# Optimization experiments

Measured on AMD Instinct MI355X. Metric: run time of the kernel, lower is better.

The kernel has to match this reference:

```python
import jax, jax.numpy as jnp
import numpy as np

B, S, E = 2, 2048, 1024
H, W_SIZE = 16, 128
D = E // H


def setup_inputs() -> dict:
    key = jax.random.key(0)
    ks = jax.random.split(key, 7)
    std = 1.0 / np.sqrt(E)
    return {
        "x": jax.random.normal(ks[0], (B, S, E), dtype=jnp.float32),
        "Wq": jax.random.normal(ks[1], (E, E), dtype=jnp.float32) * std,
        "bq": jax.random.normal(ks[2], (E,), dtype=jnp.float32) * std,
        "Wk": jax.random.normal(ks[3], (E, E), dtype=jnp.float32) * std,
        "bk": jax.random.normal(ks[4], (E,), dtype=jnp.float32) * std,
        "Wv": jax.random.normal(ks[5], (E, E), dtype=jnp.float32) * std,
        "bv": jax.random.normal(ks[6], (E,), dtype=jnp.float32) * std,
    }


def reference(x, Wq, bq, Wk, bk, Wv, bv):
    b, s, e = x.shape
    scale = jnp.float32(D) ** -0.5
    # torch Linear: y = x @ W.T + b
    # Faithful to original: view() splits [b, s, e] -> [b, H, s, D] WITHOUT transpose
    q = (x @ Wq.T + bq).reshape(b, H, s, D)
    k = (x @ Wk.T + bk).reshape(b, H, s, D)
    v = (x @ Wv.T + bv).reshape(b, H, s, D)
    # window: scores kept for j in [max(0, i - w), min(s, i + w)), zeros elsewhere
    i = jnp.arange(s)[:, None]
    j = jnp.arange(s)[None, :]
    mask = (j >= i - W_SIZE) & (j < i + W_SIZE)  # [s, s]
    qk = jnp.einsum("bhid,bhjd->bhij", q, k)
    # out-of-window entries are ZERO (not -inf) and softmax is over the full row,
    # exactly matching the original zero-padded score tensor.
    scores = jnp.where(mask, qk, 0.0) * scale
    probs = jax.nn.softmax(scores, axis=-1)
    out = jnp.einsum("bhij,bhjd->bhid", probs, v)  # [b, H, s, D]
    out = out.transpose(0, 2, 1, 3).reshape(b, s, e)
    return out
```

## Files before the change

### kernel.cpp

```cpp
#include <hip/hip_runtime.h>
#include <math.h>

#define S_LEN 2048
#define E_DIM 1024
#define NHEAD 16
#define HD 64
#define WIN 128
#define NB 2
#define MTOT (NB * S_LEN)
#define NMAT 3072

typedef float f32x4 __attribute__((ext_vector_type(4)));
typedef short bf16x8 __attribute__((ext_vector_type(8)));

#define GLOAD_LDS(g, l) __builtin_amdgcn_global_load_lds( \
    (const __attribute__((address_space(1))) unsigned int*)(g), \
    (__attribute__((address_space(3))) unsigned int*)(l), 16, 0, 0)

__device__ __forceinline__ unsigned short f2bf(float f) {
    unsigned u = __float_as_uint(f);
    u += 0x7fffu + ((u >> 16) & 1u);
    return (unsigned short)(u >> 16);
}
__device__ __forceinline__ float bf2f(unsigned short u) {
    return __uint_as_float(((unsigned)u) << 16);
}

__global__ __launch_bounds__(256) void convert_kernel(
    const float* __restrict__ x, const float* __restrict__ wq,
    const float* __restrict__ wk, const float* __restrict__ wv,
    unsigned short* __restrict__ xb, unsigned short* __restrict__ wb)
{
    const int NXQ = MTOT * E_DIM / 4;
    const int NWQ = E_DIM * E_DIM / 4;
    const int TOT = NXQ + 3 * NWQ;
    for (int i = blockIdx.x * 256 + threadIdx.x; i < TOT; i += gridDim.x * 256) {
        const float* src; unsigned short* dst; int off;
        if (i < NXQ)               { src = x;  dst = xb;                     off = i; }
        else if (i < NXQ + NWQ)    { src = wq; dst = wb;                     off = i - NXQ; }
        else if (i < NXQ + 2*NWQ)  { src = wk; dst = wb + E_DIM * E_DIM;     off = i - NXQ - NWQ; }
        else                       { src = wv; dst = wb + 2 * E_DIM * E_DIM; off = i - NXQ - 2*NWQ; }
        float4 v = ((const float4*)src)[off];
        ushort4 o;
        o.x = f2bf(v.x); o.y = f2bf(v.y); o.z = f2bf(v.z); o.w = f2bf(v.w);
        ((ushort4*)dst)[off] = o;
    }
}

__global__ __launch_bounds__(256) void gemm_mfma(
    const unsigned short* __restrict__ Ab, const unsigned short* __restrict__ Bb,
    const float* __restrict__ bq, const float* __restrict__ bk, const float* __restrict__ bv,
    unsigned short* __restrict__ Qb, unsigned short* __restrict__ Kb,
    unsigned short* __restrict__ Vb)
{
    __shared__ __align__(256) unsigned short As[128 * 64];
    __shared__ __align__(256) unsigned short Bs[128 * 64];
    const int tid  = threadIdx.x;
    const int lane = tid & 63;
    const int w    = tid >> 6;
    const int wm   = w & 1, wn = w >> 1;
    const int m0   = blockIdx.y * 128;
    const int n0   = blockIdx.x * 128;
    const int l15  = lane & 15, l4 = lane >> 4;

    f32x4 acc[16] = {};

    for (int k0 = 0; k0 < E_DIM; k0 += 64) {
        #pragma unroll
        for (int is = 0; is < 4; ++is) {
            int gid = is * 256 + tid;
            int r = gid >> 3, sl = gid & 7;
            int gran = sl ^ (r & 7);
            int wbs = is * 256 + (tid & 192);
            GLOAD_LDS(Ab + (size_t)(m0 + r) * E_DIM + k0 + gran * 8, As + wbs * 8);
            GLOAD_LDS(Bb + (size_t)(n0 + r) * E_DIM + k0 + gran * 8, Bs + wbs * 8);
        }
        __syncthreads();
        #pragma unroll
        for (int kk = 0; kk < 2; ++kk) {
            bf16x8 af[4], bfr[4];
            int sa = (kk * 4 + l4) ^ (l15 & 7);
            #pragma unroll
            for (int t = 0; t < 4; ++t) {
                int ra = wm * 64 + t * 16 + l15;
                af[t]  = *(const bf16x8*)&As[ra * 64 + sa * 8];
                int rb = wn * 64 + t * 16 + l15;
                bfr[t] = *(const bf16x8*)&Bs[rb * 64 + sa * 8];
            }
            #pragma unroll
            for (int mt = 0; mt < 4; ++mt)
                #pragma unroll
                for (int nt = 0; nt < 4; ++nt)
                    acc[mt * 4 + nt] = __builtin_amdgcn_mfma_f32_16x16x32_bf16(
                        af[mt], bfr[nt], acc[mt * 4 + nt], 0, 0, 0);
        }
        __syncthreads();
    }

    const int sel = n0 >> 10;
    const float* bias = (sel == 0) ? bq : ((sel == 1) ? bk : bv);
    unsigned short* Yb = (sel == 0) ? Qb : ((sel == 1) ? Kb : Vb);
    const int nbase = (n0 & 1023) + wn * 64;
    #pragma unroll
    for (int mt = 0; mt < 4; ++mt) {
        #pragma unroll
        for (int nt = 0; nt < 4; ++nt) {
            int n = nbase + nt * 16 + l15;
            int c = n >> 6, d = n & 63;
            float bb = bias[n];
            #pragma unroll
            for (int r = 0; r < 4; ++r) {
                int m = m0 + wm * 64 + mt * 16 + l4 * 4 + r;
                int b = m >> 11, s = m & 2047;
                int h = s >> 7;
                int i = ((s & 127) << 4) + c;
                Yb[(((size_t)(b * 16 + h) * S_LEN + i) << 6) + d] =
                    f2bf(acc[mt * 4 + nt][r] + bb);
            }
        }
    }
}

__global__ __launch_bounds__(256) void vtot_part_kernel(
    const unsigned short* __restrict__ Vb, float* __restrict__ vtp)
{
    const int bh = blockIdx.x, seg = blockIdx.y;
    const int d = threadIdx.x & 63, sl = threadIdx.x >> 6;
    const unsigned short* p = Vb + ((size_t)bh * S_LEN + seg * 256 + sl * 64) * HD + d;
    float s = 0.f;
    #pragma unroll 8
    for (int j = 0; j < 64; ++j) s += bf2f(p[(size_t)j * HD]);
    __shared__ float red[4][64];
    red[sl][d] = s;
    __syncthreads();
    if (sl == 0)
        vtp[(seg * NB * NHEAD + bh) * HD + d] = red[0][d] + red[1][d] + red[2][d] + red[3][d];
}

__global__ __launch_bounds__(256) void attn_mfma(
    const unsigned short* __restrict__ Qb, const unsigned short* __restrict__ Kb,
    const unsigned short* __restrict__ Vb, const float* __restrict__ vtp,
    float* __restrict__ out)
{
    __shared__ __align__(256) unsigned short qps[9216];
    __shared__ __align__(256) unsigned short ks[2][64 * 64];
    __shared__ __align__(256) unsigned short vts[64 * 64];
    __shared__ __align__(256) unsigned short vscr[64 * 64];

    const int qt = blockIdx.x, bh = blockIdx.y;
    const int b = bh >> 4, h = bh & 15;
    const int i0 = qt * 128;
    const int tid = threadIdx.x;
    const int w = tid >> 6, lane = tid & 63;
    const int l15 = lane & 15, quad = lane >> 4;

    const unsigned short* Qp = Qb + (size_t)bh * S_LEN * HD;
    const unsigned short* Kp = Kb + (size_t)bh * S_LEN * HD;
    const unsigned short* Vp = Vb + (size_t)bh * S_LEN * HD;

    #pragma unroll
    for (int it = 0; it < 4; ++it) {
        int gid = it * 256 + tid;
        int r = gid >> 3, sl = gid & 7;
        int gran = sl ^ (r & 7);
        int wbs = it * 256 + (tid & 192);
        GLOAD_LDS(Qp + (size_t)(i0 + r) * HD + gran * 8, qps + wbs * 8);
    }

    const int j_begin = (i0 - WIN > 0) ? i0 - WIN : 0;
    const int j_end   = (i0 + 256 < S_LEN) ? i0 + 256 : S_LEN;
    const int n_ch    = (j_end - j_begin) >> 6;

    #pragma unroll
    for (int it = 0; it < 2; ++it) {
        int gid = it * 256 + tid;
        int r = gid >> 3, sl = gid & 7;
        int gran = sl ^ (r & 7);
        int wbs = it * 256 + (tid & 192);
        GLOAD_LDS(Kp + (size_t)(j_begin + r) * HD + gran * 8, ks[0] + wbs * 8);
        GLOAD_LDS(Vp + (size_t)(j_begin + r) * HD + gran * 8, vscr + wbs * 8);
    }
    __syncthreads();

    bf16x8 aq[2][2];
    #pragma unroll
    for (int q2 = 0; q2 < 2; ++q2) {
        int row = w * 32 + q2 * 16 + l15;
        aq[q2][0] = *(const bf16x8*)&qps[(row * 8 + (quad ^ (row & 7))) * 8];
        aq[q2][1] = *(const bf16x8*)&qps[(row * 8 + ((4 + quad) ^ (row & 7))) * 8];
    }
    bf16x8 bones;
    #pragma unroll
    for (int t = 0; t < 8; ++t) bones[t] = (short)0x3F80;

    f32x4 acc_o[2][4] = {};
    f32x4 acc_sum[2] = {};
    unsigned short* psw = qps + w * 2304;

    const int td = tid & 63;
    const int toct = tid >> 6;

    for (int c = 0; c < n_ch; ++c) {
        const int cb = c & 1;
        const int jc0 = j_begin + c * 64;

        #pragma unroll
        for (int pc = 0; pc < 2; ++pc) {
            int oct = toct + pc * 4;
            bf16x8 vv;
            #pragma unroll
            for (int t = 0; t < 8; ++t)
                vv[t] = (short)vscr[(oct * 8 + t) * 64 + (((td >> 3) ^ t) * 8) + (td & 7)];
            *(bf16x8*)&vts[td * 64 + ((oct ^ (td & 7)) * 8)] = vv;
        }
        __syncthreads();

        if (c + 1 < n_ch) {
            const int jn0 = jc0 + 64;
            #pragma unroll
            for (int it = 0; it < 2; ++it) {
                int gid = it * 256 + tid;
                int r = gid >> 3, sl = gid & 7;
                int gran = sl ^ (r & 7);
                int wbs = it * 256 + (tid & 192);
                GLOAD_LDS(Kp + (size_t)(jn0 + r) * HD + gran * 8, ks[1 - cb] + wbs * 8);
                GLOAD_LDS(Vp + (size_t)(jn0 + r) * HD + gran * 8, vscr + wbs * 8);
            }
        }

        f32x4 sacc[2][4] = {};
        const unsigned short* kb = ks[cb];
        #pragma unroll
        for (int kk = 0; kk < 2; ++kk) {
            #pragma unroll
            for (int jt = 0; jt < 4; ++jt) {
                int row = jt * 16 + l15;
                bf16x8 bk = *(const bf16x8*)&kb[(row * 8 + ((kk * 4 + quad) ^ (row & 7))) * 8];
                sacc[0][jt] = __builtin_amdgcn_mfma_f32_16x16x32_bf16(aq[0][kk], bk, sacc[0][jt], 0, 0, 0);
                sacc[1][jt] = __builtin_amdgcn_mfma_f32_16x16x32_bf16(aq[1][kk], bk, sacc[1][jt], 0, 0, 0);
            }
        }

        #pragma unroll
        for (int q2 = 0; q2 < 2; ++q2) {
            #pragma unroll
            for (int jt = 0; jt < 4; ++jt) {
                int jg = jc0 + jt * 16 + l15;
                #pragma unroll
                for (int reg = 0; reg < 4; ++reg) {
                    int i = i0 + w * 32 + q2 * 16 + quad * 4 + reg;
                    bool valid = (jg >= i - WIN) && (jg < i + WIN);
                    float p = valid ? __expf(sacc[q2][jt][reg] * 0.125f) - 1.f : 0.f;
                    psw[(q2 * 16 + quad * 4 + reg) * 72 + jt * 16 + l15] = f2bf(p);
                }
            }
        }
        bf16x8 ap[2][2];
        #pragma unroll
        for (int q2 = 0; q2 < 2; ++q2) {
            ap[q2][0] = *(const bf16x8*)&psw[(q2 * 16 + l15) * 72 + quad * 8];
            ap[q2][1] = *(const bf16x8*)&psw[(q2 * 16 + l15) * 72 + 32 + quad * 8];
        }

        #pragma unroll
        for (int kst = 0; kst < 2; ++kst) {
            #pragma unroll
            for (int dt = 0; dt < 4; ++dt) {
                int row = dt * 16 + l15;
                bf16x8 bv_ = *(const bf16x8*)&vts[(row * 8 + ((kst * 4 + quad) ^ (row & 7))) * 8];
                acc_o[0][dt] = __builtin_amdgcn_mfma_f32_16x16x32_bf16(ap[0][kst], bv_, acc_o[0][dt], 0, 0, 0);
                acc_o[1][dt] = __builtin_amdgcn_mfma_f32_16x16x32_bf16(ap[1][kst], bv_, acc_o[1][dt], 0, 0, 0);
            }
            acc_sum[0] = __builtin_amdgcn_mfma_f32_16x16x32_bf16(ap[0][kst], bones, acc_sum[0], 0, 0, 0);
            acc_sum[1] = __builtin_amdgcn_mfma_f32_16x16x32_bf16(ap[1][kst], bones, acc_sum[1], 0, 0, 0);
        }
        __syncthreads();
    }

    float vtv[4];
    #pragma unroll
    for (int dt = 0; dt < 4; ++dt) {
        float s = 0.f;
        #pragma unroll
        for (int sg = 0; sg < 8; ++sg)
            s += vtp[(sg * NB * NHEAD + bh) * HD + dt * 16 + l15];
        vtv[dt] = s;
    }
    #pragma unroll
    for (int q2 = 0; q2 < 2; ++q2) {
        #pragma unroll
        for (int reg = 0; reg < 4; ++reg) {
            int i = i0 + w * 32 + q2 * 16 + quad * 4 + reg;
            float inv = 1.f / (acc_sum[q2][reg] + (float)S_LEN);
            float* op = out + (((size_t)(b * S_LEN + i)) * NHEAD + h) * HD;
            #pragma unroll
            for (int dt = 0; dt < 4; ++dt)
                op[dt * 16 + l15] = (acc_o[q2][dt][reg] + vtv[dt]) * inv;
        }
    }
}

extern "C" void kernel_launch(void* const* d_in, const int* in_sizes, int n_in,
                              void* d_out, int out_size, void* d_ws, size_t ws_size,
                              hipStream_t stream)
{
    const float* x  = (const float*)d_in[0];
    const float* Wq = (const float*)d_in[1];
    const float* bq = (const float*)d_in[2];
    const float* Wk = (const float*)d_in[3];
    const float* bk = (const float*)d_in[4];
    const float* Wv = (const float*)d_in[5];
    const float* bv = (const float*)d_in[6];
    float* out = (float*)d_out;

    const size_t NY = (size_t)MTOT * E_DIM;
    unsigned short* xb  = (unsigned short*)d_ws;
    unsigned short* wb  = xb + NY;
    unsigned short* Qb  = wb + (size_t)3 * E_DIM * E_DIM;
    unsigned short* Kb  = Qb + NY;
    unsigned short* Vb  = Kb + NY;
    float* vtp = (float*)(Vb + NY);

    convert_kernel<<<1792, 256, 0, stream>>>(x, Wq, Wk, Wv, xb, wb);
    gemm_mfma<<<dim3(NMAT / 128, MTOT / 128), 256, 0, stream>>>(xb, wb, bq, bk, bv, Qb, Kb, Vb);
    vtot_part_kernel<<<dim3(NB * NHEAD, 8), 256, 0, stream>>>(Vb, vtp);
    attn_mfma<<<dim3(S_LEN / 128, NB * NHEAD), 256, 0, stream>>>(Qb, Kb, Vb, vtp, out);
}
```

Measured before the change: 152.5 us.

## Shrink attention query tile to 64 rows and register-prefetch K/V chunks

```diff
diff --git a/kernel.cpp b/kernel.cpp
--- a/kernel.cpp
+++ b/kernel.cpp
@@ -16,6 +16,9 @@
 #define GLOAD_LDS(g, l) __builtin_amdgcn_global_load_lds( \
     (const __attribute__((address_space(1))) unsigned int*)(g), \
     (__attribute__((address_space(3))) unsigned int*)(l), 16, 0, 0)
+
+#define BAR_LDS() do { asm volatile("s_waitcnt lgkmcnt(0)" ::: "memory"); \
+                       __builtin_amdgcn_s_barrier(); } while (0)
 
 __device__ __forceinline__ unsigned short f2bf(float f) {
     unsigned u = __float_as_uint(f);
@@ -142,139 +145,139 @@
     const unsigned short* __restrict__ Vb, const float* __restrict__ vtp,
     float* __restrict__ out)
 {
-    __shared__ __align__(256) unsigned short qps[9216];
-    __shared__ __align__(256) unsigned short ks[2][64 * 64];
+    __shared__ __align__(256) unsigned short qs[64 * 64];
+    __shared__ __align__(256) unsigned short ks[64 * 64];
     __shared__ __align__(256) unsigned short vts[64 * 64];
-    __shared__ __align__(256) unsigned short vscr[64 * 64];
+    __shared__ __align__(16)  unsigned short ps[4][16 * 72];
 
     const int qt = blockIdx.x, bh = blockIdx.y;
     const int b = bh >> 4, h = bh & 15;
-    const int i0 = qt * 128;
+    const int i0 = qt * 64;
     const int tid = threadIdx.x;
     const int w = tid >> 6, lane = tid & 63;
     const int l15 = lane & 15, quad = lane >> 4;
 
+    const int lr = tid >> 2;
+    const int lg = tid & 3;
+    const int d0 = lg * 16;
+    const int keyr = lr & 7;
+    const int g0 = lg * 2;
+    const int oct = lr >> 3, jin = lr & 7;
+
     const unsigned short* Qp = Qb + (size_t)bh * S_LEN * HD;
     const unsigned short* Kp = Kb + (size_t)bh * S_LEN * HD;
     const unsigned short* Vp = Vb + (size_t)bh * S_LEN * HD;
 
-    #pragma unroll
-    for (int it = 0; it < 4; ++it) {
-        int gid = it * 256 + tid;
-        int r = gid >> 3, sl = gid & 7;
-        int gran = sl ^ (r & 7);
-        int wbs = it * 256 + (tid & 192);
-        GLOAD_LDS(Qp + (size_t)(i0 + r) * HD + gran * 8, qps + wbs * 8);
-    }
-
     const int j_begin = (i0 - WIN > 0) ? i0 - WIN : 0;
-    const int j_end   = (i0 + 256 < S_LEN) ? i0 + 256 : S_LEN;
+    const int j_end   = (i0 + 64 + WIN < S_LEN) ? i0 + 64 + WIN : S_LEN;
     const int n_ch    = (j_end - j_begin) >> 6;
 
-    #pragma unroll
-    for (int it = 0; it < 2; ++it) {
-        int gid = it * 256 + tid;
-        int r = gid >> 3, sl = gid & 7;
-        int gran = sl ^ (r & 7);
-        int wbs = it * 256 + (tid & 192);
-        GLOAD_LDS(Kp + (size_t)(j_begin + r) * HD + gran * 8, ks[0] + wbs * 8);
-        GLOAD_LDS(Vp + (size_t)(j_begin + r) * HD + gran * 8, vscr + wbs * 8);
-    }
-    __syncthreads();
-
-    bf16x8 aq[2][2];
-    #pragma unroll
-    for (int q2 = 0; q2 < 2; ++q2) {
-        int row = w * 32 + q2 * 16 + l15;
-        aq[q2][0] = *(const bf16x8*)&qps[(row * 8 + (quad ^ (row & 7))) * 8];
-        aq[q2][1] = *(const bf16x8*)&qps[(row * 8 + ((4 + quad) ^ (row & 7))) * 8];
+    uint4 qlo = *(const uint4*)&Qp[(size_t)(i0 + lr) * HD + d0];
+    uint4 qhi = *(const uint4*)&Qp[(size_t)(i0 + lr) * HD + d0 + 8];
+    uint4 klo[2], khi[2], vlo[2], vhi[2];
+    klo[0] = *(const uint4*)&Kp[(size_t)(j_begin + lr) * HD + d0];
+    khi[0] = *(const uint4*)&Kp[(size_t)(j_begin + lr) * HD + d0 + 8];
+    vlo[0] = *(const uint4*)&Vp[(size_t)(j_begin + lr) * HD + d0];
+    vhi[0] = *(const uint4*)&Vp[(size_t)(j_begin + lr) * HD + d0 + 8];
+    if (n_ch > 1) {
+        klo[1] = *(const uint4*)&Kp[(size_t)(j_begin + 64 + lr) * HD + d0];
+        khi[1] = *(const uint4*)&Kp[(size_t)(j_begin + 64 + lr) * HD + d0 + 8];
+        vlo[1] = *(const uint4*)&Vp[(size_t)(j_begin + 64 + lr) * HD + d0];
+        vhi[1] = *(const uint4*)&Vp[(size_t)(j_begin + 64 + lr) * HD + d0 + 8];
+    }
+
+    *(uint4*)&qs[lr * 64 + (g0 ^ keyr) * 8]       = qlo;
+    *(uint4*)&qs[lr * 64 + ((g0 + 1) ^ keyr) * 8] = qhi;
+    *(uint4*)&ks[lr * 64 + (g0 ^ keyr) * 8]       = klo[0];
+    *(uint4*)&ks[lr * 64 + ((g0 + 1) ^ keyr) * 8] = khi[0];
+    {
+        const unsigned short* plo = (const unsigned short*)&vlo[0];
+        const unsigned short* phi = (const unsigned short*)&vhi[0];
+        #pragma unroll
+        for (int dd = 0; dd < 8; ++dd) {
+            vts[(d0 + dd) * 64 + (oct ^ dd) * 8 + jin]     = plo[dd];
+            vts[(d0 + 8 + dd) * 64 + (oct ^ dd) * 8 + jin] = phi[dd];
+        }
+    }
+    BAR_LDS();
+
+    bf16x8 aq[2];
+    {
+        int row = w * 16 + l15;
+        aq[0] = *(const bf16x8*)&qs[(row * 8 + (quad ^ (row & 7))) * 8];
+        aq[1] = *(const bf16x8*)&qs[(row * 8 + ((4 + quad) ^ (row & 7))) * 8];
     }
     bf16x8 bones;
     #pragma unroll
     for (int t = 0; t < 8; ++t) bones[t] = (short)0x3F80;
 
-    f32x4 acc_o[2][4] = {};
-    f32x4 acc_sum[2] = {};
-    unsigned short* psw = qps + w * 2304;
-
-    const int td = tid & 63;
-    const int toct = tid >> 6;
+    f32x4 acc_o[4] = {};
+    f32x4 acc_sum = {};
+    unsigned short* psw = &ps[w][0];
 
     for (int c = 0; c < n_ch; ++c) {
         const int cb = c & 1;
         const int jc0 = j_begin + c * 64;
 
-        #pragma unroll
-        for (int pc = 0; pc < 2; ++pc) {
-            int oct = toct + pc * 4;
-            bf16x8 vv;
-            #pragma unroll
-            for (int t = 0; t < 8; ++t)
-                vv[t] = (short)vscr[(oct * 8 + t) * 64 + (((td >> 3) ^ t) * 8) + (td & 7)];
-            *(bf16x8*)&vts[td * 64 + ((oct ^ (td & 7)) * 8)] = vv;
-        }
-        __syncthreads();
-
-        if (c + 1 < n_ch) {
-            const int jn0 = jc0 + 64;
-            #pragma unroll
-            for (int it = 0; it < 2; ++it) {
-                int gid = it * 256 + tid;
-                int r = gid >> 3, sl = gid & 7;
-                int gran = sl ^ (r & 7);
-                int wbs = it * 256 + (tid & 192);
-                GLOAD_LDS(Kp + (size_t)(jn0 + r) * HD + gran * 8, ks[1 - cb] + wbs * 8);
-                GLOAD_LDS(Vp + (size_t)(jn0 + r) * HD + gran * 8, vscr + wbs * 8);
-            }
-        }
-
-        f32x4 sacc[2][4] = {};
-        const unsigned short* kb = ks[cb];
+        if (c >= 1) {
+            *(uint4*)&ks[lr * 64 + (g0 ^ keyr) * 8]       = klo[cb];
+            *(uint4*)&ks[lr * 64 + ((g0 + 1) ^ keyr) * 8] = khi[cb];
+            const unsigned short* plo = (const unsigned short*)&vlo[cb];
+            const unsigned short* phi = (const unsigned short*)&vhi[cb];
+            #pragma unroll
+            for (int dd = 0; dd < 8; ++dd) {
+                vts[(d0 + dd) * 64 + (oct ^ dd) * 8 + jin]     = plo[dd];
+                vts[(d0 + 8 + dd) * 64 + (oct ^ dd) * 8 + jin] = phi[dd];
+            }
+            BAR_LDS();
+        }
+
+        if (c + 2 < n_ch) {
+            const int jn = j_begin + (c + 2) * 64 + lr;
+            klo[cb] = *(const uint4*)&Kp[(size_t)jn * HD + d0];
+            khi[cb] = *(const uint4*)&Kp[(size_t)jn * HD + d0 + 8];
+            vlo[cb] = *(const uint4*)&Vp[(size_t)jn * HD + d0];
+            vhi[cb] = *(const uint4*)&Vp[(size_t)jn * HD + d0 + 8];
+        }
+
+        f32x4 sacc[4] = {};
         #pragma unroll
         for (int kk = 0; kk < 2; ++kk) {
             #pragma unroll
             for (int jt = 0; jt < 4; ++jt) {
                 int row = jt * 16 + l15;
-                bf16x8 bk = *(const bf16x8*)&kb[(row * 8 + ((kk * 4 + quad) ^ (row & 7))) * 8];
-                sacc[0][jt] = __builtin_amdgcn_mfma_f32_16x16x32_bf16(aq[0][kk], bk, sacc[0][jt], 0, 0, 0);
-                sacc[1][jt] = __builtin_amdgcn_mfma_f32_16x16x32_bf16(aq[1][kk], bk, sacc[1][jt], 0, 0, 0);
-            }
-        }
-
-        #pragma unroll
-        for (int q2 = 0; q2 < 2; ++q2) {
-            #pragma unroll
-            for (int jt = 0; jt < 4; ++jt) {
-                int jg = jc0 + jt * 16 + l15;
-                #pragma unroll
-                for (int reg = 0; reg < 4; ++reg) {
-                    int i = i0 + w * 32 + q2 * 16 + quad * 4 + reg;
-                    bool valid = (jg >= i - WIN) && (jg < i + WIN);
-                    float p = valid ? __expf(sacc[q2][jt][reg] * 0.125f) - 1.f : 0.f;
-                    psw[(q2 * 16 + quad * 4 + reg) * 72 + jt * 16 + l15] = f2bf(p);
-                }
-            }
-        }
-        bf16x8 ap[2][2];
-        #pragma unroll
-        for (int q2 = 0; q2 < 2; ++q2) {
-            ap[q2][0] = *(const bf16x8*)&psw[(q2 * 16 + l15) * 72 + quad * 8];
-            ap[q2][1] = *(const bf16x8*)&psw[(q2 * 16 + l15) * 72 + 32 + quad * 8];
-        }
+                bf16x8 bk = *(const bf16x8*)&ks[(row * 8 + ((kk * 4 + quad) ^ (row & 7))) * 8];
+                sacc[jt] = __builtin_amdgcn_mfma_f32_16x16x32_bf16(aq[kk], bk, sacc[jt], 0, 0, 0);
+            }
+        }
+
+        #pragma unroll
+        for (int jt = 0; jt < 4; ++jt) {
+            int jg = jc0 + jt * 16 + l15;
+            #pragma unroll
+            for (int reg = 0; reg < 4; ++reg) {
+                int i = i0 + w * 16 + quad * 4 + reg;
+                bool valid = (jg >= i - WIN) && (jg < i + WIN);
+                float p = valid ? __expf(sacc[jt][reg] * 0.125f) - 1.f : 0.f;
+                psw[(quad * 4 + reg) * 72 + jt * 16 + l15] = f2bf(p);
+            }
+        }
+        bf16x8 ap0 = *(const bf16x8*)&psw[l15 * 72 + quad * 8];
+        bf16x8 ap1 = *(const bf16x8*)&psw[l15 * 72 + 32 + quad * 8];
 
         #pragma unroll
         for (int kst = 0; kst < 2; ++kst) {
+            bf16x8 ap = kst ? ap1 : ap0;
             #pragma unroll
             for (int dt = 0; dt < 4; ++dt) {
                 int row = dt * 16 + l15;
                 bf16x8 bv_ = *(const bf16x8*)&vts[(row * 8 + ((kst * 4 + quad) ^ (row & 7))) * 8];
-                acc_o[0][dt] = __builtin_amdgcn_mfma_f32_16x16x32_bf16(ap[0][kst], bv_, acc_o[0][dt], 0, 0, 0);
-                acc_o[1][dt] = __builtin_amdgcn_mfma_f32_16x16x32_bf16(ap[1][kst], bv_, acc_o[1][dt], 0, 0, 0);
-            }
-            acc_sum[0] = __builtin_amdgcn_mfma_f32_16x16x32_bf16(ap[0][kst], bones, acc_sum[0], 0, 0, 0);
-            acc_sum[1] = __builtin_amdgcn_mfma_f32_16x16x32_bf16(ap[1][kst], bones, acc_sum[1], 0, 0, 0);
-        }
-        __syncthreads();
+                acc_o[dt] = __builtin_amdgcn_mfma_f32_16x16x32_bf16(ap, bv_, acc_o[dt], 0, 0, 0);
+            }
+            acc_sum = __builtin_amdgcn_mfma_f32_16x16x32_bf16(ap, bones, acc_sum, 0, 0, 0);
+        }
+
+        if (c + 1 < n_ch) BAR_LDS();
     }
 
     float vtv[4];
@@ -287,16 +290,13 @@
         vtv[dt] = s;
     }
     #pragma unroll
-    for (int q2 = 0; q2 < 2; ++q2) {
-        #pragma unroll
-        for (int reg = 0; reg < 4; ++reg) {
-            int i = i0 + w * 32 + q2 * 16 + quad * 4 + reg;
-            float inv = 1.f / (acc_sum[q2][reg] + (float)S_LEN);
-            float* op = out + (((size_t)(b * S_LEN + i)) * NHEAD + h) * HD;
-            #pragma unroll
-            for (int dt = 0; dt < 4; ++dt)
-                op[dt * 16 + l15] = (acc_o[q2][dt][reg] + vtv[dt]) * inv;
-        }
+    for (int reg = 0; reg < 4; ++reg) {
+        int i = i0 + w * 16 + quad * 4 + reg;
+        float inv = 1.f / (acc_sum[reg] + (float)S_LEN);
+        float* op = out + (((size_t)(b * S_LEN + i)) * NHEAD + h) * HD;
+        #pragma unroll
+        for (int dt = 0; dt < 4; ++dt)
+            op[dt * 16 + l15] = (acc_o[dt][reg] + vtv[dt]) * inv;
     }
 }
 
@@ -324,5 +324,5 @@
     convert_kernel<<<1792, 256, 0, stream>>>(x, Wq, Wk, Wv, xb, wb);
     gemm_mfma<<<dim3(NMAT / 128, MTOT / 128), 256, 0, stream>>>(xb, wb, bq, bk, bv, Qb, Kb, Vb);
     vtot_part_kernel<<<dim3(NB * NHEAD, 8), 256, 0, stream>>>(Vb, vtp);
-    attn_mfma<<<dim3(S_LEN / 128, NB * NHEAD), 256, 0, stream>>>(Qb, Kb, Vb, vtp, out);
-}
+    attn_mfma<<<dim3(S_LEN / 64, NB * NHEAD), 256, 0, stream>>>(Qb, Kb, Vb, vtp, out);
+}
```

Measured after the change: 173.4 us. 13.7% more time.

## Register-prefetch K/V two chunks ahead and remap attention blocks across heads

Applied to the files above, without the earlier changes.

```diff
diff --git a/kernel.cpp b/kernel.cpp
--- a/kernel.cpp
+++ b/kernel.cpp
@@ -16,6 +16,9 @@
 #define GLOAD_LDS(g, l) __builtin_amdgcn_global_load_lds( \
     (const __attribute__((address_space(1))) unsigned int*)(g), \
     (__attribute__((address_space(3))) unsigned int*)(l), 16, 0, 0)
+
+#define BAR_LDS() do { asm volatile("s_waitcnt lgkmcnt(0)" ::: "memory"); \
+                       __builtin_amdgcn_s_barrier(); } while (0)
 
 __device__ __forceinline__ unsigned short f2bf(float f) {
     unsigned u = __float_as_uint(f);
@@ -142,52 +145,67 @@
     const unsigned short* __restrict__ Vb, const float* __restrict__ vtp,
     float* __restrict__ out)
 {
-    __shared__ __align__(256) unsigned short qps[9216];
+    __shared__ __align__(256) unsigned short qs[128 * 64];
     __shared__ __align__(256) unsigned short ks[2][64 * 64];
+    __shared__ __align__(256) unsigned short vscr[2][64 * 64];
     __shared__ __align__(256) unsigned short vts[64 * 64];
-    __shared__ __align__(256) unsigned short vscr[64 * 64];
-
-    const int qt = blockIdx.x, bh = blockIdx.y;
+    __shared__ __align__(16)  unsigned short ps[4][32 * 72];
+
+    const int x = blockIdx.x;
+    const int bh = (x & 7) * 4 + (x >> 7);
+    const int qt = (x >> 3) & 15;
     const int b = bh >> 4, h = bh & 15;
     const int i0 = qt * 128;
     const int tid = threadIdx.x;
     const int w = tid >> 6, lane = tid & 63;
     const int l15 = lane & 15, quad = lane >> 4;
 
+    const int lr = tid >> 2;
+    const int lg = tid & 3;
+    const int d0 = lg * 16;
+    const int keyr = lr & 7;
+    const int g0 = lg * 2;
+    const int td = tid & 63;
+    const int toct = tid >> 6;
+
     const unsigned short* Qp = Qb + (size_t)bh * S_LEN * HD;
     const unsigned short* Kp = Kb + (size_t)bh * S_LEN * HD;
     const unsigned short* Vp = Vb + (size_t)bh * S_LEN * HD;
 
-    #pragma unroll
-    for (int it = 0; it < 4; ++it) {
-        int gid = it * 256 + tid;
-        int r = gid >> 3, sl = gid & 7;
-        int gran = sl ^ (r & 7);
-        int wbs = it * 256 + (tid & 192);
-        GLOAD_LDS(Qp + (size_t)(i0 + r) * HD + gran * 8, qps + wbs * 8);
-    }
-
     const int j_begin = (i0 - WIN > 0) ? i0 - WIN : 0;
-    const int j_end   = (i0 + 256 < S_LEN) ? i0 + 256 : S_LEN;
+    const int j_end   = (i0 + 128 + WIN < S_LEN) ? i0 + 128 + WIN : S_LEN;
     const int n_ch    = (j_end - j_begin) >> 6;
 
-    #pragma unroll
-    for (int it = 0; it < 2; ++it) {
-        int gid = it * 256 + tid;
-        int r = gid >> 3, sl = gid & 7;
-        int gran = sl ^ (r & 7);
-        int wbs = it * 256 + (tid & 192);
-        GLOAD_LDS(Kp + (size_t)(j_begin + r) * HD + gran * 8, ks[0] + wbs * 8);
-        GLOAD_LDS(Vp + (size_t)(j_begin + r) * HD + gran * 8, vscr + wbs * 8);
-    }
-    __syncthreads();
+    uint4 q0lo = *(const uint4*)&Qp[(size_t)(i0 + lr) * HD + d0];
+    uint4 q0hi = *(const uint4*)&Qp[(size_t)(i0 + lr) * HD + d0 + 8];
+    uint4 q1lo = *(const uint4*)&Qp[(size_t)(i0 + 64 + lr) * HD + d0];
+    uint4 q1hi = *(const uint4*)&Qp[(size_t)(i0 + 64 + lr) * HD + d0 + 8];
+    uint4 klo[2], khi[2], vlo[2], vhi[2];
+    #pragma unroll
+    for (int sl2 = 0; sl2 < 2; ++sl2) {
+        const int jr = j_begin + sl2 * 64 + lr;
+        klo[sl2] = *(const uint4*)&Kp[(size_t)jr * HD + d0];
+        khi[sl2] = *(const uint4*)&Kp[(size_t)jr * HD + d0 + 8];
+        vlo[sl2] = *(const uint4*)&Vp[(size_t)jr * HD + d0];
+        vhi[sl2] = *(const uint4*)&Vp[(size_t)jr * HD + d0 + 8];
+    }
+
+    *(uint4*)&qs[lr * 64 + (g0 ^ keyr) * 8]              = q0lo;
+    *(uint4*)&qs[lr * 64 + ((g0 + 1) ^ keyr) * 8]        = q0hi;
+    *(uint4*)&qs[(64 + lr) * 64 + (g0 ^ keyr) * 8]       = q1lo;
+    *(uint4*)&qs[(64 + lr) * 64 + ((g0 + 1) ^ keyr) * 8] = q1hi;
+    *(uint4*)&ks[0][lr * 64 + (g0 ^ keyr) * 8]           = klo[0];
+    *(uint4*)&ks[0][lr * 64 + ((g0 + 1) ^ keyr) * 8]     = khi[0];
+    *(uint4*)&vscr[0][lr * 64 + (g0 ^ keyr) * 8]         = vlo[0];
+    *(uint4*)&vscr[0][lr * 64 + ((g0 + 1) ^ keyr) * 8]   = vhi[0];
+    BAR_LDS();
 
     bf16x8 aq[2][2];
     #pragma unroll
     for (int q2 = 0; q2 < 2; ++q2) {
         int row = w * 32 + q2 * 16 + l15;
-        aq[q2][0] = *(const bf16x8*)&qps[(row * 8 + (quad ^ (row & 7))) * 8];
-        aq[q2][1] = *(const bf16x8*)&qps[(row * 8 + ((4 + quad) ^ (row & 7))) * 8];
+        aq[q2][0] = *(const bf16x8*)&qs[(row * 8 + (quad ^ (row & 7))) * 8];
+        aq[q2][1] = *(const bf16x8*)&qs[(row * 8 + ((4 + quad) ^ (row & 7))) * 8];
     }
     bf16x8 bones;
     #pragma unroll
@@ -195,10 +213,7 @@
 
     f32x4 acc_o[2][4] = {};
     f32x4 acc_sum[2] = {};
-    unsigned short* psw = qps + w * 2304;
-
-    const int td = tid & 63;
-    const int toct = tid >> 6;
+    unsigned short* psw = &ps[w][0];
 
     for (int c = 0; c < n_ch; ++c) {
         const int cb = c & 1;
@@ -210,22 +225,23 @@
             bf16x8 vv;
             #pragma unroll
             for (int t = 0; t < 8; ++t)
-                vv[t] = (short)vscr[(oct * 8 + t) * 64 + (((td >> 3) ^ t) * 8) + (td & 7)];
+                vv[t] = (short)vscr[cb][(oct * 8 + t) * 64 + (((td >> 3) ^ t) * 8) + (td & 7)];
             *(bf16x8*)&vts[td * 64 + ((oct ^ (td & 7)) * 8)] = vv;
         }
-        __syncthreads();
+        BAR_LDS();
 
         if (c + 1 < n_ch) {
-            const int jn0 = jc0 + 64;
-            #pragma unroll
-            for (int it = 0; it < 2; ++it) {
-                int gid = it * 256 + tid;
-                int r = gid >> 3, sl = gid & 7;
-                int gran = sl ^ (r & 7);
-                int wbs = it * 256 + (tid & 192);
-                GLOAD_LDS(Kp + (size_t)(jn0 + r) * HD + gran * 8, ks[1 - cb] + wbs * 8);
-                GLOAD_LDS(Vp + (size_t)(jn0 + r) * HD + gran * 8, vscr + wbs * 8);
-            }
+            *(uint4*)&ks[1 - cb][lr * 64 + (g0 ^ keyr) * 8]         = klo[1 - cb];
+            *(uint4*)&ks[1 - cb][lr * 64 + ((g0 + 1) ^ keyr) * 8]   = khi[1 - cb];
+            *(uint4*)&vscr[1 - cb][lr * 64 + (g0 ^ keyr) * 8]       = vlo[1 - cb];
+            *(uint4*)&vscr[1 - cb][lr * 64 + ((g0 + 1) ^ keyr) * 8] = vhi[1 - cb];
+        }
+        if (c + 2 < n_ch) {
+            const int jr = j_begin + (c + 2) * 64 + lr;
+            klo[cb] = *(const uint4*)&Kp[(size_t)jr * HD + d0];
+            khi[cb] = *(const uint4*)&Kp[(size_t)jr * HD + d0 + 8];
+            vlo[cb] = *(const uint4*)&Vp[(size_t)jr * HD + d0];
+            vhi[cb] = *(const uint4*)&Vp[(size_t)jr * HD + d0 + 8];
         }
 
         f32x4 sacc[2][4] = {};
@@ -274,7 +290,8 @@
             acc_sum[0] = __builtin_amdgcn_mfma_f32_16x16x32_bf16(ap[0][kst], bones, acc_sum[0], 0, 0, 0);
             acc_sum[1] = __builtin_amdgcn_mfma_f32_16x16x32_bf16(ap[1][kst], bones, acc_sum[1], 0, 0, 0);
         }
-        __syncthreads();
+
+        BAR_LDS();
     }
 
     float vtv[4];
@@ -324,5 +341,5 @@
     convert_kernel<<<1792, 256, 0, stream>>>(x, Wq, Wk, Wv, xb, wb);
     gemm_mfma<<<dim3(NMAT / 128, MTOT / 128), 256, 0, stream>>>(xb, wb, bq, bk, bv, Qb, Kb, Vb);
     vtot_part_kernel<<<dim3(NB * NHEAD, 8), 256, 0, stream>>>(Vb, vtp);
-    attn_mfma<<<dim3(S_LEN / 128, NB * NHEAD), 256, 0, stream>>>(Qb, Kb, Vb, vtp, out);
-}
+    attn_mfma<<<512, 256, 0, stream>>>(Qb, Kb, Vb, vtp, out);
+}
```

New measurement: 164.3 us. 1.08x slower.
